# Performance work log

Hardware: AMD Instinct MI355X
Metric: run time of the kernel (lower is better)

Reference implementation:

```python
import jax, jax.numpy as jnp
import numpy as np
from jax import lax

E = 5      # num experts
K = 3      # used (top-k)
B, C, H, W = 16, 128, 64, 64
DW = 2 * C   # NAFBlock DW_Expand=2
FFN = 2 * C  # NAFBlock FFN_Expand=2
EPS = 1e-6   # NAFNet LayerNorm2d eps


def setup_inputs() -> dict:
    key = jax.random.key(0)
    ks = jax.random.split(key, 12)
    r = lambda i, shape, s=0.05: jax.random.normal(ks[i], shape, jnp.float32) * s
    return dict(
        feat=jax.random.normal(ks[0], (B, C, H, W), jnp.float32),
        weights=jax.random.uniform(ks[1], (B, E), jnp.float32, minval=0.01, maxval=1.0),
        ln1_w=jnp.ones((E, C), jnp.float32), ln1_b=jnp.zeros((E, C), jnp.float32),
        conv1_w=r(2, (E, DW, C)), conv1_b=jnp.zeros((E, DW), jnp.float32),
        conv2_w=r(3, (E, DW, 1, 3, 3)), conv2_b=jnp.zeros((E, DW), jnp.float32),
        sca_w=r(4, (E, C, C)), sca_b=jnp.zeros((E, C), jnp.float32),
        conv3_w=r(5, (E, C, C)), conv3_b=jnp.zeros((E, C), jnp.float32),
        ln2_w=jnp.ones((E, C), jnp.float32), ln2_b=jnp.zeros((E, C), jnp.float32),
        conv4_w=r(6, (E, FFN, C)), conv4_b=jnp.zeros((E, FFN), jnp.float32),
        conv5_w=r(7, (E, C, FFN // 2)), conv5_b=jnp.zeros((E, C), jnp.float32),
        beta=r(8, (E, C), 1.0), gamma=r(9, (E, C), 1.0),
    )


def _ln2d(x, w, b):
    # channel-wise LayerNorm over C for each (b, h, w)
    mu = jnp.mean(x, 1, keepdims=True)
    v = jnp.mean((x - mu) ** 2, 1, keepdims=True)
    return (x - mu) * lax.rsqrt(v + EPS) * w[None, :, None, None] + b[None, :, None, None]


def _c1x1(x, w, b):
    return jnp.einsum('oc,bchw->bohw', w, x) + b[None, :, None, None]


def _sg(x):  # SimpleGate
    a, g = jnp.split(x, 2, axis=1)
    return a * g


def _naf(x, ln1w, ln1b, w1, b1, w2, b2, scaw, scab, w3, b3, ln2w, ln2b, w4, b4, w5, b5, beta, gamma):
    y = _c1x1(_ln2d(x, ln1w, ln1b), w1, b1)                      # [B,2C,H,W]
    y = lax.conv_general_dilated(y, w2, (1, 1), 'SAME',
                                 feature_group_count=DW,
                                 dimension_numbers=('NCHW', 'OIHW', 'NCHW')) + b2[None, :, None, None]
    y = _sg(y)                                                    # [B,C,H,W]
    s = jnp.einsum('oc,bc->bo', scaw, jnp.mean(y, (2, 3))) + scab # SCA
    y = y * s[:, :, None, None]
    y = _c1x1(y, w3, b3)
    x = x + y * beta[None, :, None, None]
    z = _c1x1(_sg(_c1x1(_ln2d(x, ln2w, ln2b), w4, b4)), w5, b5)
    return x + z * gamma[None, :, None, None]


def reference(feat, weights, ln1_w, ln1_b, conv1_w, conv1_b, conv2_w, conv2_b,
              sca_w, sca_b, conv3_w, conv3_b, ln2_w, ln2_b, conv4_w, conv4_b,
              conv5_w, conv5_b, beta, gamma):
    b = feat.shape[0]
    tw, ti = lax.top_k(weights, K)
    tw = tw / jnp.sum(tw, 1, keepdims=True)
    # gate[b,e] = normalized topk weight if expert e selected for sample b, else 0
    gate = jnp.zeros((b, E), feat.dtype).at[jnp.arange(b)[:, None], ti].set(tw)
    counts = jnp.bincount(ti.ravel(), length=E)
    expert_outs = jax.vmap(lambda *p: _naf(feat, *p))(
        ln1_w, ln1_b, conv1_w, conv1_b, conv2_w, conv2_b, sca_w, sca_b,
        conv3_w, conv3_b, ln2_w, ln2_b, conv4_w, conv4_b, conv5_w, conv5_b, beta, gamma)
    outputs = jnp.einsum('ebchw,be->bchw', expert_outs, gate)
    return (outputs, counts, weights)
```

## Files before the change

### kernel.cpp

```cpp
#include <hip/hip_runtime.h>

#define EN 5
#define KT 3
#define BB 16
#define CC 128
#define HWP 4096
#define DWC 256
#define NPAIR 48
#define EPSLN 1e-6f
#define HR 10
#define HPX 100
#define TSTRIDE 106

typedef float f32x4 __attribute__((ext_vector_type(4)));
typedef __bf16 bf16x8 __attribute__((ext_vector_type(8)));

__device__ __forceinline__ float bf2f(ushort u) {
  union { unsigned int u; float f; } v; v.u = ((unsigned int)u) << 16; return v.f;
}
__device__ __forceinline__ uint cvtpk(float lo, float hi) {
  uint r;
  asm("v_cvt_pk_bf16_f32 %0, %1, %2" : "=v"(r) : "v"(lo), "v"(hi));
  return r;
}
__device__ __forceinline__ ushort f2bf(float f) {
  union { float f; unsigned int u; } v; v.f = f;
  unsigned int r = v.u + 0x7FFFu + ((v.u >> 16) & 1u);
  return (ushort)(r >> 16);
}
__device__ __forceinline__ ushort f2bf1(float f) {
  return (ushort)(cvtpk(f, f) & 0xffffu);
}
__device__ __forceinline__ ushort4 pack4(float a, float b, float c, float d) {
  union { uint2 u; ushort4 s; } v;
  v.u.x = cvtpk(a, b);
  v.u.y = cvtpk(c, d);
  return v.s;
}

__global__ void gate_kernel(const float* __restrict__ weights, float* __restrict__ gate_w,
                            int* __restrict__ pair_e, float* __restrict__ out_counts,
                            float* __restrict__ out_weights, float* __restrict__ mean_raw) {
  __shared__ int sel[NPAIR];
  int tid = threadIdx.x;
  if (tid < BB) {
    float w[EN];
    for (int e = 0; e < EN; e++) w[e] = weights[tid * EN + e];
    int ch[KT]; float cv[KT]; float sum = 0.f;
    for (int j = 0; j < KT; j++) {
      int best = -1; float bv = -3.4e38f;
      for (int e = 0; e < EN; e++) {
        bool used = false;
        for (int q = 0; q < j; q++) if (ch[q] == e) used = true;
        if (!used && w[e] > bv) { bv = w[e]; best = e; }
      }
      ch[j] = best; cv[j] = bv; sum += bv;
    }
    float inv = 1.f / sum;
    for (int j = 0; j < KT; j++) {
      gate_w[tid * KT + j] = cv[j] * inv;
      pair_e[tid * KT + j] = ch[j];
      sel[tid * KT + j] = ch[j];
    }
  }
  for (int i = tid; i < NPAIR * CC; i += 256) mean_raw[i] = 0.f;
  __syncthreads();
  if (tid < EN) {
    int cnt = 0;
    for (int i = 0; i < NPAIR; i++) if (sel[i] == tid) cnt++;
    out_counts[tid] = (float)cnt;
  }
  if (tid < BB * EN) out_weights[tid] = weights[tid];
}

__global__ void fold_kernel(const float* __restrict__ conv1_w, const float* __restrict__ conv1_b,
                            const float* __restrict__ ln1_w, const float* __restrict__ ln1_b,
                            const float* __restrict__ conv4_w, const float* __restrict__ conv4_b,
                            const float* __restrict__ ln2_w, const float* __restrict__ ln2_b,
                            const float* __restrict__ conv3_b, const float* __restrict__ beta,
                            ushort* __restrict__ W1eff, float* __restrict__ b1eff,
                            ushort* __restrict__ W4eff, float* __restrict__ b4eff,
                            float* __restrict__ b3eff) {
  int gid = blockIdx.x * 256 + threadIdx.x;
  if (gid < 2 * EN * DWC) {
    int which = gid / (EN * DWC), rem = gid % (EN * DWC);
    int e = rem / DWC, o = rem % DWC;
    const float* src = (which ? conv4_w : conv1_w) + (size_t)(e * DWC + o) * CC;
    const float* lw = (which ? ln2_w : ln1_w) + e * CC;
    const float* lb = (which ? ln2_b : ln1_b) + e * CC;
    float bacc = (which ? conv4_b : conv1_b)[e * DWC + o];
    ushort* dst = (which ? W4eff : W1eff) + (size_t)(e * DWC + o) * CC;
    for (int c = 0; c < CC; c++) {
      float wv = src[c];
      dst[c] = f2bf(wv * lw[c]);
      bacc += wv * lb[c];
    }
    (which ? b4eff : b1eff)[e * DWC + o] = bacc;
  } else if (gid < 2 * EN * DWC + EN * CC) {
    int x = gid - 2 * EN * DWC;
    b3eff[x] = beta[x] * conv3_b[x];
  }
}

__global__ void fold2_kernel(const float* __restrict__ conv5_w, const float* __restrict__ conv5_b,
                             const float* __restrict__ gamma, const float* __restrict__ gate_w,
                             const int* __restrict__ pair_e,
                             ushort* __restrict__ W5eff, float* __restrict__ b5tot) {
  int gid = blockIdx.x * 256 + threadIdx.x;
  const int nW = NPAIR * CC * CC / 8;
  if (gid < nW) {
    int base = gid * 8;
    int p = base >> 14, rem = base & 16383;
    int o = rem >> 7, k0 = rem & 127;
    int e = pair_e[p];
    float sc = gamma[e * CC + o] * gate_w[p];
    const float* src = conv5_w + ((size_t)e * CC + o) * CC + k0;
    ushort* dst = W5eff + ((size_t)p * CC + o) * CC + k0;
    for (int q = 0; q < 8; q++) dst[q] = f2bf(src[q] * sc);
  } else if (gid < nW + BB * CC) {
    int x = gid - nW;
    int b = x >> 7, o = x & 127;
    float s = 0.f;
    for (int j = 0; j < KT; j++) {
      int p = b * KT + j, e = pair_e[p];
      s += gate_w[p] * gamma[e * CC + o] * conv5_b[e * CC + o];
    }
    b5tot[x] = s;
  }
}

__global__ __launch_bounds__(256) void ln1_kernel(const float* __restrict__ feat,
                                                  ushort* __restrict__ xhatT,
                                                  ushort* __restrict__ featT) {
  __shared__ float tile[CC * 64];
  __shared__ float pS[4][64], pS2[4][64], bcM[64], bcR[64];
  int bimg = blockIdx.x >> 6;
  int n0 = (blockIdx.x & 63) * 64;
  int tid = threadIdx.x;
  const float* src = feat + (size_t)bimg * CC * HWP + n0;
#pragma unroll
  for (int i = 0; i < 8; i++) {
    int ch = tid + i * 256;
    int row = ch >> 4, c16 = ch & 15;
    *(float4*)&tile[row * 64 + c16 * 4] = *(const float4*)(src + (size_t)row * HWP + c16 * 4);
  }
  __syncthreads();
  int lane = tid & 63, w = tid >> 6;
  float s = 0.f, s2 = 0.f;
#pragma unroll
  for (int i = 0; i < 32; i++) {
    float v = tile[(w * 32 + i) * 64 + lane];
    s += v; s2 += v * v;
  }
  pS[w][lane] = s; pS2[w][lane] = s2;
  __syncthreads();
  if (w == 0) {
    float t1 = pS[0][lane] + pS[1][lane] + pS[2][lane] + pS[3][lane];
    float t2 = pS2[0][lane] + pS2[1][lane] + pS2[2][lane] + pS2[3][lane];
    float mu = t1 * (1.f / CC);
    float var = t2 * (1.f / CC) - mu * mu;
    bcM[lane] = mu; bcR[lane] = rsqrtf(var + EPSLN);
  }
  __syncthreads();
  float mu = bcM[lane], r = bcR[lane];
  size_t obase = ((size_t)bimg * HWP + n0 + lane) * CC + w * 32;
#pragma unroll
  for (int i = 0; i < 4; i++) {
    float v[8];
#pragma unroll
    for (int q = 0; q < 8; q++) v[q] = tile[(w * 32 + i * 8 + q) * 64 + lane];
    *(ushort4*)(featT + obase + i * 8)     = pack4(v[0], v[1], v[2], v[3]);
    *(ushort4*)(featT + obase + i * 8 + 4) = pack4(v[4], v[5], v[6], v[7]);
    *(ushort4*)(xhatT + obase + i * 8)     = pack4((v[0]-mu)*r, (v[1]-mu)*r, (v[2]-mu)*r, (v[3]-mu)*r);
    *(ushort4*)(xhatT + obase + i * 8 + 4) = pack4((v[4]-mu)*r, (v[5]-mu)*r, (v[6]-mu)*r, (v[7]-mu)*r);
  }
}

__device__ __forceinline__ void stage_tile(const ushort* __restrict__ g, ushort* lds, int tid) {
#pragma unroll
  for (int i = 0; i < 8; i++) {
    int d = (tid + i * 256) * 16;
    int row = d >> 8;
    uint4 v = *(const uint4*)((const char*)g + d);
    *(uint4*)((char*)lds + (d ^ ((row & 7) << 4))) = v;
  }
}
__device__ __forceinline__ bf16x8 ldfrag(const ushort* lds, int row, int kb) {
  return *(const bf16x8*)((const char*)lds + row * 256 + (kb ^ ((row & 7) << 4)));
}
__device__ __forceinline__ void stage8(ushort* st, int px, int o, ushort4 v) {
  *(ushort4*)((char*)st + px * 256 + ((o * 2) ^ ((px & 7) << 4))) = v;
}
__device__ __forceinline__ uint4 ldstage16(const ushort* st, int px, int ck) {
  return *(const uint4*)((const char*)st + px * 256 + ((ck * 16) ^ ((px & 7) << 4)));
}

__global__ __launch_bounds__(256, 3) void c1dw_kernel(
    const ushort* __restrict__ W1eff, const float* __restrict__ b1eff,
    const ushort* __restrict__ xhatT,
    const float* __restrict__ conv2_w, const float* __restrict__ conv2_b,
    const int* __restrict__ pair_e, int pair_lo,
    ushort* __restrict__ yT, float* __restrict__ mean_raw) {
  __shared__ __align__(16) char smem[DWC * TSTRIDE * 2];
  int ts = blockIdx.x;
  int pc = blockIdx.z, p = pair_lo + pc, e = pair_e[p];
  int img = p / KT;
  int th = (ts >> 3) * 8, tw = (ts & 7) * 8;
  int tid = threadIdx.x, lane = tid & 63, w = tid >> 6;
  int fr = lane & 15, qf = lane >> 4;

#pragma unroll
  for (int i = 0; i < 7; i++) {
    int idx = tid + i * 256;
    if (idx < HPX * 16) {
      int r = idx >> 4, seg = idx & 15;
      int hy = r / HR, hx = r - hy * HR;
      int hh = th + hy - 1, ww = tw + hx - 1;
      int hc = min(max(hh, 0), 63), wc = min(max(ww, 0), 63);
      uint4 v = *(const uint4*)(xhatT + ((size_t)img * HWP + hc * 64 + wc) * CC + seg * 8);
      *(uint4*)(smem + r * 256 + ((seg * 16) ^ ((r & 7) << 4))) = v;
    }
  }
  __syncthreads();

  f32x4 acc[7][4] = {};
#pragma unroll
  for (int ks = 0; ks < 4; ks++) {
    bf16x8 bfr[4];
#pragma unroll
    for (int mf = 0; mf < 4; mf++)
      bfr[mf] = *(const bf16x8*)(W1eff + (size_t)(e * DWC + w * 64 + mf * 16 + fr) * CC + ks * 32 + qf * 8);
#pragma unroll
    for (int nf = 0; nf < 7; nf++) {
      bf16x8 a = ldfrag((const ushort*)smem, nf * 16 + fr, ks * 64 + qf * 16);
#pragma unroll
      for (int mf = 0; mf < 4; mf++)
        acc[nf][mf] = __builtin_amdgcn_mfma_f32_16x16x32_bf16(a, bfr[mf], acc[nf][mf], 0, 0, 0);
    }
  }
  float bias[4];
#pragma unroll
  for (int mf = 0; mf < 4; mf++) bias[mf] = b1eff[e * DWC + w * 64 + mf * 16 + fr];
  __syncthreads();

  ushort* Th = (ushort*)smem;
  int px0q = qf * 4;
#pragma unroll
  for (int nf = 0; nf < 7; nf++) {
    int px = nf * 16 + px0q;
    if (px < HPX) {
#pragma unroll
      for (int mf = 0; mf < 4; mf++) {
        int ch = w * 64 + mf * 16 + fr;
        f32x4 v = acc[nf][mf];
        float bb = bias[mf];
        uint u0 = cvtpk(v.x + bb, v.y + bb);
        uint u1 = cvtpk(v.z + bb, v.w + bb);
        ushort* dst = Th + ch * TSTRIDE + px;
        *(uint*)dst = u0;
        *(uint*)(dst + 2) = u1;
      }
    }
  }
  __syncthreads();

  int cp = tid & 127, ph2 = tid >> 7;
  bool zTop = (ph2 == 0) && (th == 0);
  bool zBot = (ph2 == 1) && (th == 56);
  bool leftE = (tw == 0), rightE = (tw == 56);
  const float* wAp = conv2_w + ((size_t)e * DWC + cp) * 9;
  const float* wGp = conv2_w + ((size_t)(e * DWC + CC) + cp) * 9;
  float wA9[9], wG9[9];
#pragma unroll
  for (int k = 0; k < 9; k++) { wA9[k] = wAp[k]; wG9[k] = wGp[k]; }
  float ba = conv2_b[e * DWC + cp], bg = conv2_b[e * DWC + CC + cp];

  auto loadrowz = [&](float* dst, const ushort* pp, bool zrow) {
    if (zrow) {
#pragma unroll
      for (int q = 0; q < 10; q++) dst[q] = 0.f;
    } else {
#pragma unroll
      for (int q = 0; q < 5; q++) {
        uint u = *(const uint*)(pp + q * 2);
        dst[q * 2]     = bf2f((ushort)(u & 0xffffu));
        dst[q * 2 + 1] = bf2f((ushort)(u >> 16));
      }
      if (leftE) dst[0] = 0.f;
      if (rightE) dst[9] = 0.f;
    }
  };
  auto comp3 = [&](const float* w9, const float* r0, const float* r1, const float* r2, float* out) {
#pragma unroll
    for (int ox = 0; ox < 8; ox++) {
      float a = r0[ox] * w9[0];
      a = fmaf(r0[ox + 1], w9[1], a); a = fmaf(r0[ox + 2], w9[2], a);
      a = fmaf(r1[ox],     w9[3], a); a = fmaf(r1[ox + 1], w9[4], a);
      a = fmaf(r1[ox + 2], w9[5], a);
      a = fmaf(r2[ox],     w9[6], a); a = fmaf(r2[ox + 1], w9[7], a);
      a = fmaf(r2[ox + 2], w9[8], a);
      out[ox] = a;
    }
  };

  float win[3][10];
  float outv[4][8];
  {
    const ushort* rA = Th + cp * TSTRIDE + ph2 * 40;
    loadrowz(win[0], rA, zTop); loadrowz(win[1], rA + 10, false); loadrowz(win[2], rA + 20, false);
    comp3(wA9, win[0], win[1], win[2], outv[0]);
    loadrowz(win[0], rA + 30, false);
    comp3(wA9, win[1], win[2], win[0], outv[1]);
    loadrowz(win[1], rA + 40, false);
    comp3(wA9, win[2], win[0], win[1], outv[2]);
    loadrowz(win[2], rA + 50, zBot);
    comp3(wA9, win[0], win[1], win[2], outv[3]);
  }
  uint ypk[16];
  float csum = 0.f;
  {
    const ushort* rG = Th + (cp + 128) * TSTRIDE + ph2 * 40;
    float gtmp[8];
    loadrowz(win[0], rG, zTop); loadrowz(win[1], rG + 10, false); loadrowz(win[2], rG + 20, false);
#pragma unroll
    for (int oy = 0; oy < 4; oy++) {
      if (oy == 1) { loadrowz(win[0], rG + 30, false); }
      if (oy == 2) { loadrowz(win[1], rG + 40, false); }
      if (oy == 3) { loadrowz(win[2], rG + 50, zBot); }
      const float* r0 = (oy == 0) ? win[0] : (oy == 1) ? win[1] : (oy == 2) ? win[2] : win[0];
      const float* r1 = (oy == 0) ? win[1] : (oy == 1) ? win[2] : (oy == 2) ? win[0] : win[1];
      const float* r2 = (oy == 0) ? win[2] : (oy == 1) ? win[0] : (oy == 2) ? win[1] : win[2];
      comp3(wG9, r0, r1, r2, gtmp);
#pragma unroll
      for (int ox = 0; ox < 8; ox += 2) {
        float y0 = (outv[oy][ox]     + ba) * (gtmp[ox]     + bg);
        float y1 = (outv[oy][ox + 1] + ba) * (gtmp[ox + 1] + bg);
        csum += y0 + y1;
        ypk[oy * 4 + (ox >> 1)] = cvtpk(y0, y1);
      }
    }
  }
  __syncthreads();

  float* psum = (float*)(smem + 16384);
#pragma unroll
  for (int oy = 0; oy < 4; oy++)
#pragma unroll
    for (int ox = 0; ox < 8; ox++) {
      int opx = (ph2 * 4 + oy) * 8 + ox;
      uint pkv = ypk[oy * 4 + (ox >> 1)];
      ushort val = (ox & 1) ? (ushort)(pkv >> 16) : (ushort)(pkv & 0xffffu);
      *(ushort*)(smem + opx * 256 + ((cp * 2) ^ ((opx & 7) << 4))) = val;
    }
  psum[tid] = csum;
  __syncthreads();
#pragma unroll
  for (int i = 0; i < 4; i++) {
    int idx = tid + i * 256;
    int opx = idx >> 4, ck = idx & 15;
    uint4 v = *(const uint4*)(smem + opx * 256 + ((ck * 16) ^ ((opx & 7) << 4)));
    int n = (th + (opx >> 3)) * 64 + tw + (opx & 7);
    *(uint4*)((char*)(yT + ((size_t)pc * HWP + n) * CC) + ck * 16) = v;
  }
  if (tid < CC) {
    atomicAdd(&mean_raw[p * CC + tid], psum[tid] + psum[CC + tid]);
  }
}

__global__ void sca_w3fold_kernel(const float* __restrict__ mean_raw,
                                  const float* __restrict__ sca_w, const float* __restrict__ sca_b,
                                  const float* __restrict__ conv3_w, const float* __restrict__ beta,
                                  const int* __restrict__ pair_e, int pair_lo,
                                  ushort* __restrict__ W3eff) {
  __shared__ float m[CC];
  __shared__ float sv[CC];
  int pc = blockIdx.x, p = pair_lo + pc, e = pair_e[p];
  int tid = threadIdx.x;
  if (tid < CC) m[tid] = mean_raw[p * CC + tid] * (1.f / HWP);
  __syncthreads();
  if (tid < CC) {
    const float* wr = sca_w + (size_t)(e * CC + tid) * CC;
    float acc = sca_b[e * CC + tid];
#pragma unroll 8
    for (int c = 0; c < CC; c++) acc = fmaf(wr[c], m[c], acc);
    sv[tid] = acc;
  }
  __syncthreads();
#pragma unroll
  for (int i = 0; i < 8; i++) {
    int idx = tid + i * 256;
    int o = idx >> 4, k0 = (idx & 15) * 8;
    float bt = beta[e * CC + o];
    const float* src = conv3_w + ((size_t)e * CC + o) * CC + k0;
    ushort* dst = W3eff + ((size_t)pc * CC + o) * CC + k0;
#pragma unroll
    for (int q = 0; q < 8; q++) dst[q] = f2bf(src[q] * sv[k0 + q] * bt);
  }
}

__global__ __launch_bounds__(256, 2) void conv3_ln2_kernel(
    const ushort* __restrict__ W3eff, const float* __restrict__ b3eff,
    const ushort* __restrict__ yT, const ushort* __restrict__ featT,
    const int* __restrict__ pair_e, int pair_lo,
    ushort* __restrict__ x1T, ushort* __restrict__ xh2T) {
  __shared__ ushort Ws[CC * CC];
  __shared__ ushort As[CC * CC];
  int pc = blockIdx.z, p = pair_lo + pc, e = pair_e[p];
  int img = p / KT;
  int n0 = blockIdx.x * 128;
  int tid = threadIdx.x, lane = tid & 63, w = tid >> 6;
  stage_tile(W3eff + (size_t)pc * CC * CC, Ws, tid);
  stage_tile(yT + ((size_t)pc * HWP + n0) * CC, As, tid);
  __syncthreads();
  int wr = w >> 1, wc = w & 1, fr = lane & 15, kb0 = (lane >> 4) * 16, og = (lane >> 4) * 4;
  f32x4 acc[4][4] = {};
#pragma unroll
  for (int ks = 0; ks < 4; ks++) {
    bf16x8 a[4], b[4];
#pragma unroll
    for (int m = 0; m < 4; m++) a[m] = ldfrag(Ws, wr * 64 + m * 16 + fr, ks * 64 + kb0);
#pragma unroll
    for (int n = 0; n < 4; n++) b[n] = ldfrag(As, wc * 64 + n * 16 + fr, ks * 64 + kb0);
#pragma unroll
    for (int m = 0; m < 4; m++)
#pragma unroll
      for (int n = 0; n < 4; n++)
        acc[m][n] = __builtin_amdgcn_mfma_f32_16x16x32_bf16(a[m], b[n], acc[m][n], 0, 0, 0);
  }
  float s[4] = {}, s2[4] = {};
#pragma unroll
  for (int m = 0; m < 4; m++) {
    int o = wr * 64 + m * 16 + og;
    float4 bvv = *(const float4*)&b3eff[e * CC + o];
#pragma unroll
    for (int n = 0; n < 4; n++) {
      int px = wc * 64 + n * 16 + fr;
      ushort4 f4 = *(const ushort4*)(featT + ((size_t)img * HWP + n0 + px) * CC + o);
      f32x4 v = acc[m][n];
      v.x += bf2f(f4.x) + bvv.x; v.y += bf2f(f4.y) + bvv.y;
      v.z += bf2f(f4.z) + bvv.z; v.w += bf2f(f4.w) + bvv.w;
      acc[m][n] = v;
      s[n] += v.x + v.y + v.z + v.w;
      s2[n] += v.x * v.x + v.y * v.y + v.z * v.z + v.w * v.w;
    }
  }
#pragma unroll
  for (int n = 0; n < 4; n++) {
    s[n] += __shfl_xor(s[n], 16, 64); s[n] += __shfl_xor(s[n], 32, 64);
    s2[n] += __shfl_xor(s2[n], 16, 64); s2[n] += __shfl_xor(s2[n], 32, 64);
  }
  __syncthreads();
  float2* red = (float2*)As;
  if (lane < 16) {
#pragma unroll
    for (int n = 0; n < 4; n++) {
      float2 v; v.x = s[n]; v.y = s2[n];
      red[wr * 128 + wc * 64 + n * 16 + fr] = v;
    }
  }
  __syncthreads();
  float mu[4], rs[4];
#pragma unroll
  for (int n = 0; n < 4; n++) {
    int px = wc * 64 + n * 16 + fr;
    float2 r0 = red[px], r1 = red[128 + px];
    float m_ = (r0.x + r1.x) * (1.f / CC);
    float var = (r0.y + r1.y) * (1.f / CC) - m_ * m_;
    mu[n] = m_; rs[n] = rsqrtf(var + EPSLN);
  }
  __syncthreads();
#pragma unroll
  for (int m = 0; m < 4; m++) {
    int o = wr * 64 + m * 16 + og;
#pragma unroll
    for (int n = 0; n < 4; n++) {
      int px = wc * 64 + n * 16 + fr;
      f32x4 v = acc[m][n];
      stage8(As, px, o, pack4(v.x, v.y, v.z, v.w));
      stage8(Ws, px, o, pack4((v.x - mu[n]) * rs[n], (v.y - mu[n]) * rs[n],
                              (v.z - mu[n]) * rs[n], (v.w - mu[n]) * rs[n]));
    }
  }
  __syncthreads();
#pragma unroll
  for (int i = 0; i < 8; i++) {
    int idx = tid + i * 256;
    int px = idx >> 4, ck = idx & 15;
    size_t gb = ((size_t)pc * HWP + n0 + px) * CC;
    *(uint4*)((char*)(x1T + gb) + ck * 16)  = ldstage16(As, px, ck);
    *(uint4*)((char*)(xh2T + gb) + ck * 16) = ldstage16(Ws, px, ck);
  }
}

__global__ __launch_bounds__(256, 2) void conv4sg_kernel(
    const ushort* __restrict__ W4eff, const float* __restrict__ b4eff,
    const ushort* __restrict__ xh2T, const int* __restrict__ pair_e,
    int pair_lo, ushort* __restrict__ g5T) {
  __shared__ ushort Ws[CC * CC];
  __shared__ ushort As[CC * CC];
  int pc = blockIdx.z, p = pair_lo + pc, e = pair_e[p];
  int n0 = blockIdx.x * 128;
  int tid = threadIdx.x, lane = tid & 63, w = tid >> 6;
  int wr = w >> 1, wc = w & 1, fr = lane & 15, kb0 = (lane >> 4) * 16, og = (lane >> 4) * 4;
  stage_tile(W4eff + (size_t)e * DWC * CC, Ws, tid);
  stage_tile(xh2T + ((size_t)pc * HWP + n0) * CC, As, tid);
  __syncthreads();
  f32x4 accA[4][4] = {}, accG[4][4] = {};
#pragma unroll
  for (int ks = 0; ks < 4; ks++) {
    bf16x8 a[4], b[4];
#pragma unroll
    for (int m = 0; m < 4; m++) a[m] = ldfrag(Ws, wr * 64 + m * 16 + fr, ks * 64 + kb0);
#pragma unroll
    for (int n = 0; n < 4; n++) b[n] = ldfrag(As, wc * 64 + n * 16 + fr, ks * 64 + kb0);
#pragma unroll
    for (int m = 0; m < 4; m++)
#pragma unroll
      for (int n = 0; n < 4; n++)
        accA[m][n] = __builtin_amdgcn_mfma_f32_16x16x32_bf16(a[m], b[n], accA[m][n], 0, 0, 0);
  }
  __syncthreads();
  stage_tile(W4eff + ((size_t)e * DWC + CC) * CC, Ws, tid);
  __syncthreads();
#pragma unroll
  for (int ks = 0; ks < 4; ks++) {
    bf16x8 a[4], b[4];
#pragma unroll
    for (int m = 0; m < 4; m++) a[m] = ldfrag(Ws, wr * 64 + m * 16 + fr, ks * 64 + kb0);
#pragma unroll
    for (int n = 0; n < 4; n++) b[n] = ldfrag(As, wc * 64 + n * 16 + fr, ks * 64 + kb0);
#pragma unroll
    for (int m = 0; m < 4; m++)
#pragma unroll
      for (int n = 0; n < 4; n++)
        accG[m][n] = __builtin_amdgcn_mfma_f32_16x16x32_bf16(a[m], b[n], accG[m][n], 0, 0, 0);
  }
  __syncthreads();
#pragma unroll
  for (int m = 0; m < 4; m++) {
    int o = wr * 64 + m * 16 + og;
    float4 ba = *(const float4*)&b4eff[e * DWC + o];
    float4 bg = *(const float4*)&b4eff[e * DWC + CC + o];
#pragma unroll
    for (int n = 0; n < 4; n++) {
      int px = wc * 64 + n * 16 + fr;
      f32x4 va = accA[m][n], vg = accG[m][n];
      stage8(Ws, px, o, pack4((va.x + ba.x) * (vg.x + bg.x), (va.y + ba.y) * (vg.y + bg.y),
                              (va.z + ba.z) * (vg.z + bg.z), (va.w + ba.w) * (vg.w + bg.w)));
    }
  }
  __syncthreads();
#pragma unroll
  for (int i = 0; i < 8; i++) {
    int idx = tid + i * 256;
    int px = idx >> 4, ck = idx & 15;
    uint4 v = ldstage16(Ws, px, ck);
    *(uint4*)((char*)(g5T + ((size_t)pc * HWP + n0 + px) * CC) + ck * 16) = v;
  }
}

__global__ __launch_bounds__(256, 2) void conv5_kernel(
    const ushort* __restrict__ W5eff, const float* __restrict__ b5tot,
    const ushort* __restrict__ g5T, const ushort* __restrict__ x1,
    const float* __restrict__ gate_w, int pair_lo, float* __restrict__ out) {
  __shared__ ushort Ws[CC * CC];
  __shared__ ushort As[CC * CC];
  int sl = blockIdx.z;
  int n0 = blockIdx.x * 128;
  int b = pair_lo / KT + sl;
  int tid = threadIdx.x, lane = tid & 63, w = tid >> 6;
  int wr = w >> 1, wc = w & 1;
  int fr = lane & 15, kb0 = (lane >> 4) * 16, og = (lane >> 4) * 4;
  f32x4 acc[4][4] = {};
  for (int j = 0; j < KT; j++) {
    int pc = sl * KT + j, p = pair_lo + pc;
    __syncthreads();
    stage_tile(W5eff + (size_t)p * CC * CC, Ws, tid);
    stage_tile(g5T + ((size_t)pc * HWP + n0) * CC, As, tid);
    __syncthreads();
#pragma unroll
    for (int ks = 0; ks < 4; ks++) {
      bf16x8 a[4], bfr[4];
#pragma unroll
      for (int m = 0; m < 4; m++) a[m] = ldfrag(Ws, wr * 64 + m * 16 + fr, ks * 64 + kb0);
#pragma unroll
      for (int n = 0; n < 4; n++) bfr[n] = ldfrag(As, wc * 64 + n * 16 + fr, ks * 64 + kb0);
#pragma unroll
      for (int m = 0; m < 4; m++)
#pragma unroll
        for (int n = 0; n < 4; n++)
          acc[m][n] = __builtin_amdgcn_mfma_f32_16x16x32_bf16(a[m], bfr[n], acc[m][n], 0, 0, 0);
    }
  }
  float gw0 = gate_w[pair_lo + sl * KT + 0];
  float gw1 = gate_w[pair_lo + sl * KT + 1];
  float gw2 = gate_w[pair_lo + sl * KT + 2];
  __syncthreads();
  ushort* Ct = As;
#pragma unroll
  for (int m = 0; m < 4; m++) {
    int o = wr * 64 + m * 16 + og;
    float4 bt = *(const float4*)&b5tot[b * CC + o];
#pragma unroll
    for (int n = 0; n < 4; n++) {
      int px = wc * 64 + n * 16 + fr;
      f32x4 v = acc[m][n];
      float r0 = v.x + bt.x, r1 = v.y + bt.y, r2 = v.z + bt.z, r3 = v.w + bt.w;
      size_t xoff = ((size_t)(sl * KT) * HWP + n0 + px) * CC + o;
      ushort4 xa = *(const ushort4*)(x1 + xoff);
      ushort4 xb = *(const ushort4*)(x1 + xoff + (size_t)HWP * CC);
      ushort4 xc = *(const ushort4*)(x1 + xoff + 2 * (size_t)HWP * CC);
      r0 += gw0 * bf2f(xa.x) + gw1 * bf2f(xb.x) + gw2 * bf2f(xc.x);
      r1 += gw0 * bf2f(xa.y) + gw1 * bf2f(xb.y) + gw2 * bf2f(xc.y);
      r2 += gw0 * bf2f(xa.z) + gw1 * bf2f(xb.z) + gw2 * bf2f(xc.z);
      r3 += gw0 * bf2f(xa.w) + gw1 * bf2f(xb.w) + gw2 * bf2f(xc.w);
      *(ushort*)((char*)Ct + (o+0) * 256 + ((px*2) ^ (((o+0) & 7) << 4))) = f2bf1(r0);
      *(ushort*)((char*)Ct + (o+1) * 256 + ((px*2) ^ (((o+1) & 7) << 4))) = f2bf1(r1);
      *(ushort*)((char*)Ct + (o+2) * 256 + ((px*2) ^ (((o+2) & 7) << 4))) = f2bf1(r2);
      *(ushort*)((char*)Ct + (o+3) * 256 + ((px*2) ^ (((o+3) & 7) << 4))) = f2bf1(r3);
    }
  }
  __syncthreads();
  int o = tid >> 1, ph = (tid & 1) * 64;
  float* orow = out + ((size_t)(b * CC + o)) * HWP + n0 + ph;
  int swz = (o & 7) << 4;
#pragma unroll
  for (int i = 0; i < 8; i++) {
    const ushort* lp = (const ushort*)((const char*)Ct + o * 256 + ((ph * 2 + i * 16) ^ swz));
    float4 f0, f1;
    f0.x = bf2f(lp[0]); f0.y = bf2f(lp[1]); f0.z = bf2f(lp[2]); f0.w = bf2f(lp[3]);
    f1.x = bf2f(lp[4]); f1.y = bf2f(lp[5]); f1.z = bf2f(lp[6]); f1.w = bf2f(lp[7]);
    *(float4*)(orow + i * 8) = f0;
    *(float4*)(orow + i * 8 + 4) = f1;
  }
}

extern "C" void kernel_launch(void* const* d_in, const int* in_sizes, int n_in,
                              void* d_out, int out_size, void* d_ws, size_t ws_size,
                              hipStream_t stream) {
  const float* feat    = (const float*)d_in[0];
  const float* weights = (const float*)d_in[1];
  const float* ln1_w   = (const float*)d_in[2];
  const float* ln1_b   = (const float*)d_in[3];
  const float* conv1_w = (const float*)d_in[4];
  const float* conv1_b = (const float*)d_in[5];
  const float* conv2_w = (const float*)d_in[6];
  const float* conv2_b = (const float*)d_in[7];
  const float* sca_w   = (const float*)d_in[8];
  const float* sca_b   = (const float*)d_in[9];
  const float* conv3_w = (const float*)d_in[10];
  const float* conv3_b = (const float*)d_in[11];
  const float* ln2_w   = (const float*)d_in[12];
  const float* ln2_b   = (const float*)d_in[13];
  const float* conv4_w = (const float*)d_in[14];
  const float* conv4_b = (const float*)d_in[15];
  const float* conv5_w = (const float*)d_in[16];
  const float* conv5_b = (const float*)d_in[17];
  const float* beta    = (const float*)d_in[18];
  const float* gamma   = (const float*)d_in[19];

  float* out = (float*)d_out;
  float* out_counts = out + (size_t)BB * CC * HWP;
  float* out_weights = out_counts + EN;

  char* base = (char*)d_ws;
  size_t off = 0;
  auto carveU = [&](size_t n) -> ushort* { ushort* p = (ushort*)(base + off); off += n * 2; return p; };
  auto carveF = [&](size_t n) -> float* { float* p = (float*)(base + off); off += n * 4; return p; };

  ushort* W1eff = carveU((size_t)EN * DWC * CC);
  ushort* W4eff = carveU((size_t)EN * DWC * CC);
  ushort* W5eff = carveU((size_t)NPAIR * CC * CC);
  ushort* W3eff = carveU((size_t)NPAIR * CC * CC);
  float* b1eff  = carveF(EN * DWC);
  float* b4eff  = carveF(EN * DWC);
  float* b3eff  = carveF(EN * CC);
  float* b5tot  = carveF(BB * CC);
  float* gate_w = carveF(64);
  int*   pair_e = (int*)carveF(64);
  float* mean_raw = carveF(NPAIR * CC);
  ushort* xhatT = carveU((size_t)BB * HWP * CC);
  ushort* featT = carveU((size_t)BB * HWP * CC);

  const size_t per_pair = (size_t)3 * HWP * CC * 2;
  int ns = 16;
  while (ns > 1 && off + (size_t)ns * KT * per_pair > ws_size) ns >>= 1;
  size_t pr = (size_t)ns * KT;
  ushort* y_T   = carveU(pr * HWP * CC);
  ushort* x1_T  = carveU(pr * HWP * CC);
  ushort* g5_T  = carveU(pr * HWP * CC);
  ushort* xh2_T = y_T;

  gate_kernel<<<1, 256, 0, stream>>>(weights, gate_w, pair_e, out_counts, out_weights, mean_raw);
  fold_kernel<<<13, 256, 0, stream>>>(conv1_w, conv1_b, ln1_w, ln1_b,
                                      conv4_w, conv4_b, ln2_w, ln2_b,
                                      conv3_b, beta, W1eff, b1eff, W4eff, b4eff, b3eff);
  fold2_kernel<<<393, 256, 0, stream>>>(conv5_w, conv5_b, gamma, gate_w, pair_e, W5eff, b5tot);
  ln1_kernel<<<BB * 64, 256, 0, stream>>>(feat, xhatT, featT);

  for (int s0 = 0; s0 < BB; s0 += ns) {
    int np = ns * KT, plo = s0 * KT;
    c1dw_kernel<<<dim3(64, 1, np), 256, 0, stream>>>(W1eff, b1eff, xhatT, conv2_w, conv2_b,
                                                     pair_e, plo, y_T, mean_raw);
    sca_w3fold_kernel<<<np, 256, 0, stream>>>(mean_raw, sca_w, sca_b, conv3_w, beta,
                                              pair_e, plo, W3eff);
    conv3_ln2_kernel<<<dim3(32, 1, np), 256, 0, stream>>>(W3eff, b3eff, y_T, featT,
                                                          pair_e, plo, x1_T, xh2_T);
    conv4sg_kernel<<<dim3(32, 1, np), 256, 0, stream>>>(W4eff, b4eff, xh2_T, pair_e, plo, g5_T);
    conv5_kernel<<<dim3(32, 1, ns), 256, 0, stream>>>(W5eff, b5tot, g5_T, x1_T,
                                                      gate_w, plo, out);
  }
}
```

Baseline: 214.2 us.

## Fuse conv3+LN2, conv4+SimpleGate and conv5 into a single per-tile kernel

Merges the conv3/LN2, conv4/SimpleGate and conv5 kernels into one naf2_kernel that loops over the three selected experts per image. Intermediates x1, xh2 and g5 stay in registers and LDS, and the gated residual is accumulated in registers instead of being written to global memory and read back. This removes two intermediate global buffers and two launches, and lets the staging batch grow. The cost is a grid of 32×ns blocks instead of 32×np, so parallelism drops by a factor of KT, and more accumulators per thread raise register pressure.

After: 249.1 us. +16.3%, slower.

```diff
diff --git a/kernel.cpp b/kernel.cpp
--- a/kernel.cpp
+++ b/kernel.cpp
@@ -191,9 +191,6 @@
 __device__ __forceinline__ void stage8(ushort* st, int px, int o, ushort4 v) {
   *(ushort4*)((char*)st + px * 256 + ((o * 2) ^ ((px & 7) << 4))) = v;
 }
-__device__ __forceinline__ uint4 ldstage16(const ushort* st, int px, int ck) {
-  return *(const uint4*)((const char*)st + px * 256 + ((ck * 16) ^ ((px & 7) << 4)));
-}
 
 __global__ __launch_bounds__(256, 3) void c1dw_kernel(
     const ushort* __restrict__ W1eff, const float* __restrict__ b1eff,
@@ -398,203 +395,178 @@
   }
 }
 
-__global__ __launch_bounds__(256, 2) void conv3_ln2_kernel(
+__global__ __launch_bounds__(256, 2) void naf2_kernel(
     const ushort* __restrict__ W3eff, const float* __restrict__ b3eff,
+    const ushort* __restrict__ W4eff, const float* __restrict__ b4eff,
+    const ushort* __restrict__ W5eff, const float* __restrict__ b5tot,
     const ushort* __restrict__ yT, const ushort* __restrict__ featT,
-    const int* __restrict__ pair_e, int pair_lo,
-    ushort* __restrict__ x1T, ushort* __restrict__ xh2T) {
-  __shared__ ushort Ws[CC * CC];
-  __shared__ ushort As[CC * CC];
-  int pc = blockIdx.z, p = pair_lo + pc, e = pair_e[p];
-  int img = p / KT;
-  int n0 = blockIdx.x * 128;
-  int tid = threadIdx.x, lane = tid & 63, w = tid >> 6;
-  stage_tile(W3eff + (size_t)pc * CC * CC, Ws, tid);
-  stage_tile(yT + ((size_t)pc * HWP + n0) * CC, As, tid);
-  __syncthreads();
-  int wr = w >> 1, wc = w & 1, fr = lane & 15, kb0 = (lane >> 4) * 16, og = (lane >> 4) * 4;
-  f32x4 acc[4][4] = {};
-#pragma unroll
-  for (int ks = 0; ks < 4; ks++) {
-    bf16x8 a[4], b[4];
-#pragma unroll
-    for (int m = 0; m < 4; m++) a[m] = ldfrag(Ws, wr * 64 + m * 16 + fr, ks * 64 + kb0);
-#pragma unroll
-    for (int n = 0; n < 4; n++) b[n] = ldfrag(As, wc * 64 + n * 16 + fr, ks * 64 + kb0);
-#pragma unroll
-    for (int m = 0; m < 4; m++)
-#pragma unroll
-      for (int n = 0; n < 4; n++)
-        acc[m][n] = __builtin_amdgcn_mfma_f32_16x16x32_bf16(a[m], b[n], acc[m][n], 0, 0, 0);
-  }
-  float s[4] = {}, s2[4] = {};
-#pragma unroll
-  for (int m = 0; m < 4; m++) {
-    int o = wr * 64 + m * 16 + og;
-    float4 bvv = *(const float4*)&b3eff[e * CC + o];
-#pragma unroll
-    for (int n = 0; n < 4; n++) {
-      int px = wc * 64 + n * 16 + fr;
-      ushort4 f4 = *(const ushort4*)(featT + ((size_t)img * HWP + n0 + px) * CC + o);
-      f32x4 v = acc[m][n];
-      v.x += bf2f(f4.x) + bvv.x; v.y += bf2f(f4.y) + bvv.y;
-      v.z += bf2f(f4.z) + bvv.z; v.w += bf2f(f4.w) + bvv.w;
-      acc[m][n] = v;
-      s[n] += v.x + v.y + v.z + v.w;
-      s2[n] += v.x * v.x + v.y * v.y + v.z * v.z + v.w * v.w;
-    }
-  }
-#pragma unroll
-  for (int n = 0; n < 4; n++) {
-    s[n] += __shfl_xor(s[n], 16, 64); s[n] += __shfl_xor(s[n], 32, 64);
-    s2[n] += __shfl_xor(s2[n], 16, 64); s2[n] += __shfl_xor(s2[n], 32, 64);
-  }
-  __syncthreads();
-  float2* red = (float2*)As;
-  if (lane < 16) {
-#pragma unroll
-    for (int n = 0; n < 4; n++) {
-      float2 v; v.x = s[n]; v.y = s2[n];
-      red[wr * 128 + wc * 64 + n * 16 + fr] = v;
-    }
-  }
-  __syncthreads();
-  float mu[4], rs[4];
-#pragma unroll
-  for (int n = 0; n < 4; n++) {
-    int px = wc * 64 + n * 16 + fr;
-    float2 r0 = red[px], r1 = red[128 + px];
-    float m_ = (r0.x + r1.x) * (1.f / CC);
-    float var = (r0.y + r1.y) * (1.f / CC) - m_ * m_;
-    mu[n] = m_; rs[n] = rsqrtf(var + EPSLN);
-  }
-  __syncthreads();
-#pragma unroll
-  for (int m = 0; m < 4; m++) {
-    int o = wr * 64 + m * 16 + og;
-#pragma unroll
-    for (int n = 0; n < 4; n++) {
-      int px = wc * 64 + n * 16 + fr;
-      f32x4 v = acc[m][n];
-      stage8(As, px, o, pack4(v.x, v.y, v.z, v.w));
-      stage8(Ws, px, o, pack4((v.x - mu[n]) * rs[n], (v.y - mu[n]) * rs[n],
-                              (v.z - mu[n]) * rs[n], (v.w - mu[n]) * rs[n]));
-    }
-  }
-  __syncthreads();
-#pragma unroll
-  for (int i = 0; i < 8; i++) {
-    int idx = tid + i * 256;
-    int px = idx >> 4, ck = idx & 15;
-    size_t gb = ((size_t)pc * HWP + n0 + px) * CC;
-    *(uint4*)((char*)(x1T + gb) + ck * 16)  = ldstage16(As, px, ck);
-    *(uint4*)((char*)(xh2T + gb) + ck * 16) = ldstage16(Ws, px, ck);
-  }
-}
-
-__global__ __launch_bounds__(256, 2) void conv4sg_kernel(
-    const ushort* __restrict__ W4eff, const float* __restrict__ b4eff,
-    const ushort* __restrict__ xh2T, const int* __restrict__ pair_e,
-    int pair_lo, ushort* __restrict__ g5T) {
-  __shared__ ushort Ws[CC * CC];
-  __shared__ ushort As[CC * CC];
-  int pc = blockIdx.z, p = pair_lo + pc, e = pair_e[p];
-  int n0 = blockIdx.x * 128;
-  int tid = threadIdx.x, lane = tid & 63, w = tid >> 6;
-  int wr = w >> 1, wc = w & 1, fr = lane & 15, kb0 = (lane >> 4) * 16, og = (lane >> 4) * 4;
-  stage_tile(W4eff + (size_t)e * DWC * CC, Ws, tid);
-  stage_tile(xh2T + ((size_t)pc * HWP + n0) * CC, As, tid);
-  __syncthreads();
-  f32x4 accA[4][4] = {}, accG[4][4] = {};
-#pragma unroll
-  for (int ks = 0; ks < 4; ks++) {
-    bf16x8 a[4], b[4];
-#pragma unroll
-    for (int m = 0; m < 4; m++) a[m] = ldfrag(Ws, wr * 64 + m * 16 + fr, ks * 64 + kb0);
-#pragma unroll
-    for (int n = 0; n < 4; n++) b[n] = ldfrag(As, wc * 64 + n * 16 + fr, ks * 64 + kb0);
-#pragma unroll
-    for (int m = 0; m < 4; m++)
-#pragma unroll
-      for (int n = 0; n < 4; n++)
-        accA[m][n] = __builtin_amdgcn_mfma_f32_16x16x32_bf16(a[m], b[n], accA[m][n], 0, 0, 0);
-  }
-  __syncthreads();
-  stage_tile(W4eff + ((size_t)e * DWC + CC) * CC, Ws, tid);
-  __syncthreads();
-#pragma unroll
-  for (int ks = 0; ks < 4; ks++) {
-    bf16x8 a[4], b[4];
-#pragma unroll
-    for (int m = 0; m < 4; m++) a[m] = ldfrag(Ws, wr * 64 + m * 16 + fr, ks * 64 + kb0);
-#pragma unroll
-    for (int n = 0; n < 4; n++) b[n] = ldfrag(As, wc * 64 + n * 16 + fr, ks * 64 + kb0);
-#pragma unroll
-    for (int m = 0; m < 4; m++)
-#pragma unroll
-      for (int n = 0; n < 4; n++)
-        accG[m][n] = __builtin_amdgcn_mfma_f32_16x16x32_bf16(a[m], b[n], accG[m][n], 0, 0, 0);
-  }
-  __syncthreads();
-#pragma unroll
-  for (int m = 0; m < 4; m++) {
-    int o = wr * 64 + m * 16 + og;
-    float4 ba = *(const float4*)&b4eff[e * DWC + o];
-    float4 bg = *(const float4*)&b4eff[e * DWC + CC + o];
-#pragma unroll
-    for (int n = 0; n < 4; n++) {
-      int px = wc * 64 + n * 16 + fr;
-      f32x4 va = accA[m][n], vg = accG[m][n];
-      stage8(Ws, px, o, pack4((va.x + ba.x) * (vg.x + bg.x), (va.y + ba.y) * (vg.y + bg.y),
-                              (va.z + ba.z) * (vg.z + bg.z), (va.w + ba.w) * (vg.w + bg.w)));
-    }
-  }
-  __syncthreads();
-#pragma unroll
-  for (int i = 0; i < 8; i++) {
-    int idx = tid + i * 256;
-    int px = idx >> 4, ck = idx & 15;
-    uint4 v = ldstage16(Ws, px, ck);
-    *(uint4*)((char*)(g5T + ((size_t)pc * HWP + n0 + px) * CC) + ck * 16) = v;
-  }
-}
-
-__global__ __launch_bounds__(256, 2) void conv5_kernel(
-    const ushort* __restrict__ W5eff, const float* __restrict__ b5tot,
-    const ushort* __restrict__ g5T, const ushort* __restrict__ x1,
-    const float* __restrict__ gate_w, int pair_lo, float* __restrict__ out) {
+    const float* __restrict__ gate_w, const int* __restrict__ pair_e, int pair_lo,
+    float* __restrict__ out) {
   __shared__ ushort Ws[CC * CC];
   __shared__ ushort As[CC * CC];
   int sl = blockIdx.z;
   int n0 = blockIdx.x * 128;
   int b = pair_lo / KT + sl;
   int tid = threadIdx.x, lane = tid & 63, w = tid >> 6;
-  int wr = w >> 1, wc = w & 1;
-  int fr = lane & 15, kb0 = (lane >> 4) * 16, og = (lane >> 4) * 4;
-  f32x4 acc[4][4] = {};
+  int wr = w >> 1, wc = w & 1, fr = lane & 15, kb0 = (lane >> 4) * 16, og = (lane >> 4) * 4;
+  f32x4 acc5[4][4] = {};
+  f32x4 xres[4][4] = {};
+
   for (int j = 0; j < KT; j++) {
-    int pc = sl * KT + j, p = pair_lo + pc;
-    __syncthreads();
+    int pc = sl * KT + j, p = pair_lo + pc, e = pair_e[p];
+    float gw = gate_w[p];
+    __syncthreads();
+    stage_tile(W3eff + (size_t)pc * CC * CC, Ws, tid);
+    stage_tile(yT + ((size_t)pc * HWP + n0) * CC, As, tid);
+    __syncthreads();
+    f32x4 acc3[4][4] = {};
+#pragma unroll
+    for (int ks = 0; ks < 4; ks++) {
+      bf16x8 a[4], bb[4];
+#pragma unroll
+      for (int m = 0; m < 4; m++) a[m] = ldfrag(Ws, wr * 64 + m * 16 + fr, ks * 64 + kb0);
+#pragma unroll
+      for (int n = 0; n < 4; n++) bb[n] = ldfrag(As, wc * 64 + n * 16 + fr, ks * 64 + kb0);
+#pragma unroll
+      for (int m = 0; m < 4; m++)
+#pragma unroll
+        for (int n = 0; n < 4; n++)
+          acc3[m][n] = __builtin_amdgcn_mfma_f32_16x16x32_bf16(a[m], bb[n], acc3[m][n], 0, 0, 0);
+    }
+    float s[4] = {}, s2[4] = {};
+#pragma unroll
+    for (int m = 0; m < 4; m++) {
+      int o = wr * 64 + m * 16 + og;
+      float4 bvv = *(const float4*)&b3eff[e * CC + o];
+#pragma unroll
+      for (int n = 0; n < 4; n++) {
+        int px = wc * 64 + n * 16 + fr;
+        ushort4 f4 = *(const ushort4*)(featT + ((size_t)b * HWP + n0 + px) * CC + o);
+        f32x4 v = acc3[m][n];
+        v.x += bf2f(f4.x) + bvv.x; v.y += bf2f(f4.y) + bvv.y;
+        v.z += bf2f(f4.z) + bvv.z; v.w += bf2f(f4.w) + bvv.w;
+        acc3[m][n] = v;
+        f32x4 xr = xres[m][n];
+        xr.x += gw * v.x; xr.y += gw * v.y; xr.z += gw * v.z; xr.w += gw * v.w;
+        xres[m][n] = xr;
+        s[n] += v.x + v.y + v.z + v.w;
+        s2[n] += v.x * v.x + v.y * v.y + v.z * v.z + v.w * v.w;
+      }
+    }
+#pragma unroll
+    for (int n = 0; n < 4; n++) {
+      s[n] += __shfl_xor(s[n], 16, 64); s[n] += __shfl_xor(s[n], 32, 64);
+      s2[n] += __shfl_xor(s2[n], 16, 64); s2[n] += __shfl_xor(s2[n], 32, 64);
+    }
+    __syncthreads();
+    float2* red = (float2*)As;
+    if (lane < 16) {
+#pragma unroll
+      for (int n = 0; n < 4; n++) {
+        float2 v; v.x = s[n]; v.y = s2[n];
+        red[wr * 128 + wc * 64 + n * 16 + fr] = v;
+      }
+    }
+    stage_tile(W4eff + (size_t)e * DWC * CC, Ws, tid);
+    __syncthreads();
+    float mu[4], rs[4];
+#pragma unroll
+    for (int n = 0; n < 4; n++) {
+      int px = wc * 64 + n * 16 + fr;
+      float2 r0 = red[px], r1 = red[128 + px];
+      float m_ = (r0.x + r1.x) * (1.f / CC);
+      float var = (r0.y + r1.y) * (1.f / CC) - m_ * m_;
+      mu[n] = m_; rs[n] = rsqrtf(var + EPSLN);
+    }
+    __syncthreads();
+#pragma unroll
+    for (int m = 0; m < 4; m++) {
+      int o = wr * 64 + m * 16 + og;
+#pragma unroll
+      for (int n = 0; n < 4; n++) {
+        int px = wc * 64 + n * 16 + fr;
+        f32x4 v = acc3[m][n];
+        stage8(As, px, o, pack4((v.x - mu[n]) * rs[n], (v.y - mu[n]) * rs[n],
+                                (v.z - mu[n]) * rs[n], (v.w - mu[n]) * rs[n]));
+      }
+    }
+    __syncthreads();
+    f32x4 accA[4][4] = {};
+#pragma unroll
+    for (int ks = 0; ks < 4; ks++) {
+      bf16x8 a[4], bb[4];
+#pragma unroll
+      for (int m = 0; m < 4; m++) a[m] = ldfrag(Ws, wr * 64 + m * 16 + fr, ks * 64 + kb0);
+#pragma unroll
+      for (int n = 0; n < 4; n++) bb[n] = ldfrag(As, wc * 64 + n * 16 + fr, ks * 64 + kb0);
+#pragma unroll
+      for (int m = 0; m < 4; m++)
+#pragma unroll
+        for (int n = 0; n < 4; n++)
+          accA[m][n] = __builtin_amdgcn_mfma_f32_16x16x32_bf16(a[m], bb[n], accA[m][n], 0, 0, 0);
+    }
+    uint pA[4][4][2];
+#pragma unroll
+    for (int m = 0; m < 4; m++) {
+      int o = wr * 64 + m * 16 + og;
+      float4 ba4 = *(const float4*)&b4eff[e * DWC + o];
+#pragma unroll
+      for (int n = 0; n < 4; n++) {
+        f32x4 v = accA[m][n];
+        pA[m][n][0] = cvtpk(v.x + ba4.x, v.y + ba4.y);
+        pA[m][n][1] = cvtpk(v.z + ba4.z, v.w + ba4.w);
+      }
+    }
+    __syncthreads();
+    stage_tile(W4eff + ((size_t)e * DWC + CC) * CC, Ws, tid);
+    __syncthreads();
+    f32x4 accG[4][4] = {};
+#pragma unroll
+    for (int ks = 0; ks < 4; ks++) {
+      bf16x8 a[4], bb[4];
+#pragma unroll
+      for (int m = 0; m < 4; m++) a[m] = ldfrag(Ws, wr * 64 + m * 16 + fr, ks * 64 + kb0);
+#pragma unroll
+      for (int n = 0; n < 4; n++) bb[n] = ldfrag(As, wc * 64 + n * 16 + fr, ks * 64 + kb0);
+#pragma unroll
+      for (int m = 0; m < 4; m++)
+#pragma unroll
+        for (int n = 0; n < 4; n++)
+          accG[m][n] = __builtin_amdgcn_mfma_f32_16x16x32_bf16(a[m], bb[n], accG[m][n], 0, 0, 0);
+    }
+    __syncthreads();
+#pragma unroll
+    for (int m = 0; m < 4; m++) {
+      int o = wr * 64 + m * 16 + og;
+      float4 bg4 = *(const float4*)&b4eff[e * DWC + CC + o];
+#pragma unroll
+      for (int n = 0; n < 4; n++) {
+        int px = wc * 64 + n * 16 + fr;
+        f32x4 vg = accG[m][n];
+        uint u0 = pA[m][n][0], u1 = pA[m][n][1];
+        float g0 = bf2f((ushort)(u0 & 0xffffu)) * (vg.x + bg4.x);
+        float g1 = bf2f((ushort)(u0 >> 16))     * (vg.y + bg4.y);
+        float g2 = bf2f((ushort)(u1 & 0xffffu)) * (vg.z + bg4.z);
+        float g3 = bf2f((ushort)(u1 >> 16))     * (vg.w + bg4.w);
+        stage8(As, px, o, pack4(g0, g1, g2, g3));
+      }
+    }
     stage_tile(W5eff + (size_t)p * CC * CC, Ws, tid);
-    stage_tile(g5T + ((size_t)pc * HWP + n0) * CC, As, tid);
     __syncthreads();
 #pragma unroll
     for (int ks = 0; ks < 4; ks++) {
-      bf16x8 a[4], bfr[4];
+      bf16x8 a[4], bb[4];
 #pragma unroll
       for (int m = 0; m < 4; m++) a[m] = ldfrag(Ws, wr * 64 + m * 16 + fr, ks * 64 + kb0);
 #pragma unroll
-      for (int n = 0; n < 4; n++) bfr[n] = ldfrag(As, wc * 64 + n * 16 + fr, ks * 64 + kb0);
+      for (int n = 0; n < 4; n++) bb[n] = ldfrag(As, wc * 64 + n * 16 + fr, ks * 64 + kb0);
 #pragma unroll
       for (int m = 0; m < 4; m++)
 #pragma unroll
         for (int n = 0; n < 4; n++)
-          acc[m][n] = __builtin_amdgcn_mfma_f32_16x16x32_bf16(a[m], bfr[n], acc[m][n], 0, 0, 0);
-    }
-  }
-  float gw0 = gate_w[pair_lo + sl * KT + 0];
-  float gw1 = gate_w[pair_lo + sl * KT + 1];
-  float gw2 = gate_w[pair_lo + sl * KT + 2];
+          acc5[m][n] = __builtin_amdgcn_mfma_f32_16x16x32_bf16(a[m], bb[n], acc5[m][n], 0, 0, 0);
+    }
+  }
   __syncthreads();
   ushort* Ct = As;
 #pragma unroll
@@ -604,16 +576,12 @@
 #pragma unroll
     for (int n = 0; n < 4; n++) {
       int px = wc * 64 + n * 16 + fr;
-      f32x4 v = acc[m][n];
-      float r0 = v.x + bt.x, r1 = v.y + bt.y, r2 = v.z + bt.z, r3 = v.w + bt.w;
-      size_t xoff = ((size_t)(sl * KT) * HWP + n0 + px) * CC + o;
-      ushort4 xa = *(const ushort4*)(x1 + xoff);
-      ushort4 xb = *(const ushort4*)(x1 + xoff + (size_t)HWP * CC);
-      ushort4 xc = *(const ushort4*)(x1 + xoff + 2 * (size_t)HWP * CC);
-      r0 += gw0 * bf2f(xa.x) + gw1 * bf2f(xb.x) + gw2 * bf2f(xc.x);
-      r1 += gw0 * bf2f(xa.y) + gw1 * bf2f(xb.y) + gw2 * bf2f(xc.y);
-      r2 += gw0 * bf2f(xa.z) + gw1 * bf2f(xb.z) + gw2 * bf2f(xc.z);
-      r3 += gw0 * bf2f(xa.w) + gw1 * bf2f(xb.w) + gw2 * bf2f(xc.w);
+      f32x4 v = acc5[m][n];
+      f32x4 xr = xres[m][n];
+      float r0 = v.x + bt.x + xr.x;
+      float r1 = v.y + bt.y + xr.y;
+      float r2 = v.z + bt.z + xr.z;
+      float r3 = v.w + bt.w + xr.w;
       *(ushort*)((char*)Ct + (o+0) * 256 + ((px*2) ^ (((o+0) & 7) << 4))) = f2bf1(r0);
       *(ushort*)((char*)Ct + (o+1) * 256 + ((px*2) ^ (((o+1) & 7) << 4))) = f2bf1(r1);
       *(ushort*)((char*)Ct + (o+2) * 256 + ((px*2) ^ (((o+2) & 7) << 4))) = f2bf1(r2);
@@ -682,14 +650,11 @@
   ushort* xhatT = carveU((size_t)BB * HWP * CC);
   ushort* featT = carveU((size_t)BB * HWP * CC);
 
-  const size_t per_pair = (size_t)3 * HWP * CC * 2;
+  const size_t per_pair = (size_t)HWP * CC * 2;
   int ns = 16;
   while (ns > 1 && off + (size_t)ns * KT * per_pair > ws_size) ns >>= 1;
   size_t pr = (size_t)ns * KT;
-  ushort* y_T   = carveU(pr * HWP * CC);
-  ushort* x1_T  = carveU(pr * HWP * CC);
-  ushort* g5_T  = carveU(pr * HWP * CC);
-  ushort* xh2_T = y_T;
+  ushort* y_T = carveU(pr * HWP * CC);
 
   gate_kernel<<<1, 256, 0, stream>>>(weights, gate_w, pair_e, out_counts, out_weights, mean_raw);
   fold_kernel<<<13, 256, 0, stream>>>(conv1_w, conv1_b, ln1_w, ln1_b,
@@ -704,10 +669,7 @@
                                                      pair_e, plo, y_T, mean_raw);
     sca_w3fold_kernel<<<np, 256, 0, stream>>>(mean_raw, sca_w, sca_b, conv3_w, beta,
                                               pair_e, plo, W3eff);
-    conv3_ln2_kernel<<<dim3(32, 1, np), 256, 0, stream>>>(W3eff, b3eff, y_T, featT,
-                                                          pair_e, plo, x1_T, xh2_T);
-    conv4sg_kernel<<<dim3(32, 1, np), 256, 0, stream>>>(W4eff, b4eff, xh2_T, pair_e, plo, g5_T);
-    conv5_kernel<<<dim3(32, 1, ns), 256, 0, stream>>>(W5eff, b5tot, g5_T, x1_T,
-                                                      gate_w, plo, out);
-  }
-}
+    naf2_kernel<<<dim3(32, 1, ns), 256, 0, stream>>>(W3eff, b3eff, W4eff, b4eff, W5eff, b5tot,
+                                                     y_T, featT, gate_w, pair_e, plo, out);
+  }
+}
```
